# Performance work log

Measured on AMD Instinct MI355X. Metric: run time of the kernel, lower is better.

Reference implementation:

```python
import jax, jax.numpy as jnp
import numpy as np

C3_CONNECTIONS = [[0, 1, 2], [1, 2, 3], [2, 3, 4], [3, 4, 5], [4, 5, 0], [5, 0, 1],
                  [0, 1, 2, 3], [1, 2, 3, 4], [2, 3, 4, 5], [3, 4, 5, 0], [4, 5, 0, 1], [5, 0, 1, 2],
                  [0, 1, 3, 4], [1, 2, 4, 5], [0, 2, 3, 5], [0, 1, 2, 3, 4, 5]]

def _connectivity_mask():
    # [16, 6, 5, 5] binary mask encoding the partial-connection table
    m = np.zeros((16, 6, 5, 5), dtype=np.float32)
    for i, conn in enumerate(C3_CONNECTIONS):
        m[i, conn] = 1.0
    return jnp.asarray(m)

MASK = _connectivity_mask()


def setup_inputs() -> dict:
    key = jax.random.key(0)
    kx, kw, kb = jax.random.split(key, 3)
    x = jax.random.normal(kx, (64, 6, 256, 256), dtype=jnp.float32)
    # full dense weight; unconnected entries are masked out inside reference(),
    # which makes the math identical to the 16 separate tiny convs
    W = jax.random.normal(kw, (16, 6, 5, 5), dtype=jnp.float32) * 0.1
    b = jax.random.normal(kb, (16,), dtype=jnp.float32) * 0.1
    return {"x": x, "W": W, "b": b}


def reference(x, W, b):
    # masked dense conv == 16 channel-subset convs concatenated on channel dim
    Wm = W * MASK
    y = jax.lax.conv_general_dilated(
        x, Wm, window_strides=(1, 1), padding='VALID',
        dimension_numbers=('NCHW', 'OIHW', 'NCHW'))
    y = y + b[None, :, None, None]  # [B, 16, 252, 252]
    return 1.7159 * jnp.tanh((2.0 / 3.0) * y)
```

## Files before the change

### kernel.cpp

```cpp
#include <hip/hip_runtime.h>


__device__ __forceinline__ void conv25(const float* __restrict__ wp,
                                       const float (&win)[6][5],
                                       float& a0, float& a1) {
    #pragma unroll
    for (int ky = 0; ky < 5; ++ky)
        #pragma unroll
        for (int kx = 0; kx < 5; ++kx) {
            const float wv = wp[ky * 5 + kx];
            a0 = fmaf(win[ky + 0][kx], wv, a0);
            a1 = fmaf(win[ky + 1][kx], wv, a1);
        }
}

__global__ __launch_bounds__(256) void c3_partial_conv_kernel(
    const float* __restrict__ x,
    const float* __restrict__ W,
    const float* __restrict__ b,
    float* __restrict__ out)
{
    constexpr int G0N[6] = {4, 5, 5, 5, 4, 3};
    constexpr int G0O[6][5] = {
        {0, 4, 5, 6, 0},
        {0, 1, 5, 6, 7},
        {0, 1, 2, 6, 7},
        {1, 2, 3, 6, 7},
        {2, 3, 4, 7, 0},
        {3, 4, 5, 0, 0}};
    constexpr int G1N[6] = {6, 5, 5, 5, 6, 7};
    constexpr int G1O[6][7] = {
        {9, 10, 11, 12, 14, 15, 8},
        {10, 11, 12, 13, 15, 8, 8},
        {8, 11, 13, 14, 15, 8, 8},
        {8, 9, 12, 14, 15, 8, 8},
        {8, 9, 10, 12, 13, 15, 8},
        {8, 9, 10, 11, 13, 14, 15}};

    __shared__ float lds[6][20][40];

    const int tx  = threadIdx.x;
    const int ty  = threadIdx.y;
    const int tid = ty * 32 + tx;

    const int tileX = blockIdx.x << 5;
    const int tileY = blockIdx.y << 4;
    const int batch = blockIdx.z;

    const float* xb = x + (size_t)batch * 6 * 256 * 256;

    for (int i = tid; i < 1080; i += 256) {
        int c   = i / 180;
        int rem = i - c * 180;
        int r   = rem / 9;
        int q   = rem - r * 9;
        int gr  = tileY + r;
        int gc0 = tileX + (q << 2);
        float4 v = make_float4(0.f, 0.f, 0.f, 0.f);
        if (gr < 256 && gc0 < 256)
            v = *reinterpret_cast<const float4*>(&xb[(c * 256 + gr) * 256 + gc0]);
        *reinterpret_cast<float4*>(&lds[c][r][q << 2]) = v;
    }
    __syncthreads();

    const int row0 = ty << 1;
    const int ocol = tileX + tx;
    float* ob = out + (size_t)batch * 16 * 252 * 252;
    const bool colok = (ocol < 252);

    {
        float acc[8][2];
        #pragma unroll
        for (int o = 0; o < 8; ++o) {
            float bv = b[o];
            acc[o][0] = bv; acc[o][1] = bv;
        }

        #pragma unroll 1
        for (int c = 0; c < 6; ++c) {
            float win[6][5];
            #pragma unroll
            for (int r = 0; r < 6; ++r)
                #pragma unroll
                for (int j = 0; j < 5; ++j) {
                    win[r][j] = lds[c][row0 + r][tx + j];
                    asm volatile("" : "+v"(win[r][j]));
                }

            const int n = G0N[c];
            #pragma unroll 1
            for (int oi = 0; oi < n; ++oi) {
                switch (G0O[c][oi]) {
                    case 0: conv25(W + (0 * 6 + c) * 25, win, acc[0][0], acc[0][1]); break;
                    case 1: conv25(W + (1 * 6 + c) * 25, win, acc[1][0], acc[1][1]); break;
                    case 2: conv25(W + (2 * 6 + c) * 25, win, acc[2][0], acc[2][1]); break;
                    case 3: conv25(W + (3 * 6 + c) * 25, win, acc[3][0], acc[3][1]); break;
                    case 4: conv25(W + (4 * 6 + c) * 25, win, acc[4][0], acc[4][1]); break;
                    case 5: conv25(W + (5 * 6 + c) * 25, win, acc[5][0], acc[5][1]); break;
                    case 6: conv25(W + (6 * 6 + c) * 25, win, acc[6][0], acc[6][1]); break;
                    case 7: conv25(W + (7 * 6 + c) * 25, win, acc[7][0], acc[7][1]); break;
                    default: break;
                }
            }
        }

        if (colok) {
            #pragma unroll
            for (int o = 0; o < 8; ++o)
                #pragma unroll
                for (int dy = 0; dy < 2; ++dy) {
                    int orow = tileY + row0 + dy;
                    if (orow < 252) {
                        float z = acc[o][dy] * (2.0f / 3.0f);
                        float e = __expf(2.0f * z);
                        float rr = __builtin_amdgcn_rcpf(e + 1.0f);
                        ob[(o * 252 + orow) * 252 + ocol] = 1.7159f * (1.0f - 2.0f * rr);
                    }
                }
        }
    }

    __builtin_amdgcn_sched_barrier(0);

    {
        float acc[8][2];
        #pragma unroll
        for (int o = 0; o < 8; ++o) {
            float bv = b[8 + o];
            acc[o][0] = bv; acc[o][1] = bv;
        }

        #pragma unroll 1
        for (int c = 0; c < 6; ++c) {
            float win[6][5];
            #pragma unroll
            for (int r = 0; r < 6; ++r)
                #pragma unroll
                for (int j = 0; j < 5; ++j) {
                    win[r][j] = lds[c][row0 + r][tx + j];
                    asm volatile("" : "+v"(win[r][j]));
                }

            const int n = G1N[c];
            #pragma unroll 1
            for (int oi = 0; oi < n; ++oi) {
                switch (G1O[c][oi]) {
                    case  8: conv25(W + ( 8 * 6 + c) * 25, win, acc[0][0], acc[0][1]); break;
                    case  9: conv25(W + ( 9 * 6 + c) * 25, win, acc[1][0], acc[1][1]); break;
                    case 10: conv25(W + (10 * 6 + c) * 25, win, acc[2][0], acc[2][1]); break;
                    case 11: conv25(W + (11 * 6 + c) * 25, win, acc[3][0], acc[3][1]); break;
                    case 12: conv25(W + (12 * 6 + c) * 25, win, acc[4][0], acc[4][1]); break;
                    case 13: conv25(W + (13 * 6 + c) * 25, win, acc[5][0], acc[5][1]); break;
                    case 14: conv25(W + (14 * 6 + c) * 25, win, acc[6][0], acc[6][1]); break;
                    case 15: conv25(W + (15 * 6 + c) * 25, win, acc[7][0], acc[7][1]); break;
                    default: break;
                }
            }
        }

        if (colok) {
            #pragma unroll
            for (int o = 0; o < 8; ++o)
                #pragma unroll
                for (int dy = 0; dy < 2; ++dy) {
                    int orow = tileY + row0 + dy;
                    if (orow < 252) {
                        float z = acc[o][dy] * (2.0f / 3.0f);
                        float e = __expf(2.0f * z);
                        float rr = __builtin_amdgcn_rcpf(e + 1.0f);
                        ob[((8 + o) * 252 + orow) * 252 + ocol] = 1.7159f * (1.0f - 2.0f * rr);
                    }
                }
        }
    }
}

extern "C" void kernel_launch(void* const* d_in, const int* in_sizes, int n_in,
                              void* d_out, int out_size, void* d_ws, size_t ws_size,
                              hipStream_t stream) {
    const float* x = (const float*)d_in[0];
    const float* W = (const float*)d_in[1];
    const float* b = (const float*)d_in[2];
    float* out = (float*)d_out;

    dim3 grid(8, 16, 64);
    dim3 block(32, 8);
    hipLaunchKernelGGL(c3_partial_conv_kernel, grid, block, 0, stream, x, W, b, out);
}
```

Baseline: 252.8 us.

## Pack row pairs in LDS and use packed FMA with duplicated weights

Shared memory now stores each input as interleaved pairs of adjacent rows (v2f). This lets each thread compute its two output rows with packed two-wide FMAs (v_pk_fma_f32) against weights that a small prep kernel duplicates and pads into a workspace. The goal is to halve the FMA instruction count and the scalar LDS reads per window. It adds a second kernel launch, a workspace dependency, doubled LDS footprint per pixel, and two accumulator chains merged at the end.

```diff
diff --git a/kernel.cpp b/kernel.cpp
--- a/kernel.cpp
+++ b/kernel.cpp
@@ -1,22 +1,33 @@
 #include <hip/hip_runtime.h>
 
 
-__device__ __forceinline__ void conv25(const float* __restrict__ wp,
-                                       const float (&win)[6][5],
-                                       float& a0, float& a1) {
+typedef float v2f __attribute__((ext_vector_type(2)));
+
+__global__ void prep_weights(const float* __restrict__ W, float* __restrict__ Wp) {
+    int i = blockIdx.x * 256 + threadIdx.x;
+    if (i < 96 * 64) {
+        int oc = i >> 6, k = i & 63;
+        Wp[i] = (k < 50) ? W[oc * 25 + (k >> 1)] : 0.0f;
+    }
+}
+
+__device__ __forceinline__ void convpk(const v2f* __restrict__ w2,
+                                       const v2f (&win)[5][5], v2f& acc) {
+    v2f t0 = acc;
+    v2f t1 = {0.0f, 0.0f};
     #pragma unroll
     for (int ky = 0; ky < 5; ++ky)
         #pragma unroll
         for (int kx = 0; kx < 5; ++kx) {
-            const float wv = wp[ky * 5 + kx];
-            a0 = fmaf(win[ky + 0][kx], wv, a0);
-            a1 = fmaf(win[ky + 1][kx], wv, a1);
-        }
+            if (ky & 1) t1 = __builtin_elementwise_fma(win[ky][kx], w2[ky * 5 + kx], t1);
+            else        t0 = __builtin_elementwise_fma(win[ky][kx], w2[ky * 5 + kx], t0);
+        }
+    acc = t0 + t1;
 }
 
 __global__ __launch_bounds__(256) void c3_partial_conv_kernel(
     const float* __restrict__ x,
-    const float* __restrict__ W,
+    const float* __restrict__ Wp,
     const float* __restrict__ b,
     float* __restrict__ out)
 {
@@ -37,7 +48,7 @@
         {8, 9, 10, 12, 13, 15, 8},
         {8, 9, 10, 11, 13, 14, 15}};
 
-    __shared__ float lds[6][20][40];
+    __shared__ v2f ldsP[6][19][40];
 
     const int tx  = threadIdx.x;
     const int ty  = threadIdx.y;
@@ -49,17 +60,25 @@
 
     const float* xb = x + (size_t)batch * 6 * 256 * 256;
 
-    for (int i = tid; i < 1080; i += 256) {
-        int c   = i / 180;
-        int rem = i - c * 180;
-        int r   = rem / 9;
-        int q   = rem - r * 9;
-        int gr  = tileY + r;
+    for (int i = tid; i < 1026; i += 256) {
+        int c   = i / 171;
+        int rem = i - c * 171;
+        int pr  = rem / 9;
+        int q   = rem - pr * 9;
+        int gr  = tileY + pr;
         int gc0 = tileX + (q << 2);
-        float4 v = make_float4(0.f, 0.f, 0.f, 0.f);
-        if (gr < 256 && gc0 < 256)
-            v = *reinterpret_cast<const float4*>(&xb[(c * 256 + gr) * 256 + gc0]);
-        *reinterpret_cast<float4*>(&lds[c][r][q << 2]) = v;
+        float4 a = make_float4(0.f, 0.f, 0.f, 0.f);
+        float4 d = make_float4(0.f, 0.f, 0.f, 0.f);
+        if (gc0 < 256) {
+            const float* rowp = &xb[(c * 256 + gr) * 256 + gc0];
+            if (gr < 256)     a = *reinterpret_cast<const float4*>(rowp);
+            if (gr + 1 < 256) d = *reinterpret_cast<const float4*>(rowp + 256);
+        }
+        v2f* dst = &ldsP[c][pr][q << 2];
+        dst[0] = v2f{a.x, d.x};
+        dst[1] = v2f{a.y, d.y};
+        dst[2] = v2f{a.z, d.z};
+        dst[3] = v2f{a.w, d.w};
     }
     __syncthreads();
 
@@ -67,38 +86,36 @@
     const int ocol = tileX + tx;
     float* ob = out + (size_t)batch * 16 * 252 * 252;
     const bool colok = (ocol < 252);
+    const v2f* w2base = reinterpret_cast<const v2f*>(Wp);
 
     {
-        float acc[8][2];
+        v2f accp[8];
         #pragma unroll
-        for (int o = 0; o < 8; ++o) {
-            float bv = b[o];
-            acc[o][0] = bv; acc[o][1] = bv;
-        }
+        for (int o = 0; o < 8; ++o) { float bv = b[o]; accp[o] = v2f{bv, bv}; }
 
         #pragma unroll 1
         for (int c = 0; c < 6; ++c) {
-            float win[6][5];
-            #pragma unroll
-            for (int r = 0; r < 6; ++r)
-                #pragma unroll
-                for (int j = 0; j < 5; ++j) {
-                    win[r][j] = lds[c][row0 + r][tx + j];
-                    asm volatile("" : "+v"(win[r][j]));
-                }
+            v2f win[5][5];
+            const v2f* cb = &ldsP[c][row0][tx];
+            #pragma unroll
+            for (int ky = 0; ky < 5; ++ky)
+                #pragma unroll
+                for (int kx = 0; kx < 5; ++kx)
+                    win[ky][kx] = cb[ky * 40 + kx];
 
             const int n = G0N[c];
             #pragma unroll 1
             for (int oi = 0; oi < n; ++oi) {
-                switch (G0O[c][oi]) {
-                    case 0: conv25(W + (0 * 6 + c) * 25, win, acc[0][0], acc[0][1]); break;
-                    case 1: conv25(W + (1 * 6 + c) * 25, win, acc[1][0], acc[1][1]); break;
-                    case 2: conv25(W + (2 * 6 + c) * 25, win, acc[2][0], acc[2][1]); break;
-                    case 3: conv25(W + (3 * 6 + c) * 25, win, acc[3][0], acc[3][1]); break;
-                    case 4: conv25(W + (4 * 6 + c) * 25, win, acc[4][0], acc[4][1]); break;
-                    case 5: conv25(W + (5 * 6 + c) * 25, win, acc[5][0], acc[5][1]); break;
-                    case 6: conv25(W + (6 * 6 + c) * 25, win, acc[6][0], acc[6][1]); break;
-                    case 7: conv25(W + (7 * 6 + c) * 25, win, acc[7][0], acc[7][1]); break;
+                const int o = G0O[c][oi];
+                switch (o) {
+                    case 0: convpk(w2base + (0 * 6 + c) * 32, win, accp[0]); break;
+                    case 1: convpk(w2base + (1 * 6 + c) * 32, win, accp[1]); break;
+                    case 2: convpk(w2base + (2 * 6 + c) * 32, win, accp[2]); break;
+                    case 3: convpk(w2base + (3 * 6 + c) * 32, win, accp[3]); break;
+                    case 4: convpk(w2base + (4 * 6 + c) * 32, win, accp[4]); break;
+                    case 5: convpk(w2base + (5 * 6 + c) * 32, win, accp[5]); break;
+                    case 6: convpk(w2base + (6 * 6 + c) * 32, win, accp[6]); break;
+                    case 7: convpk(w2base + (7 * 6 + c) * 32, win, accp[7]); break;
                     default: break;
                 }
             }
@@ -106,53 +123,52 @@
 
         if (colok) {
             #pragma unroll
-            for (int o = 0; o < 8; ++o)
+            for (int o = 0; o < 8; ++o) {
+                float av[2] = {accp[o].x, accp[o].y};
                 #pragma unroll
                 for (int dy = 0; dy < 2; ++dy) {
                     int orow = tileY + row0 + dy;
                     if (orow < 252) {
-                        float z = acc[o][dy] * (2.0f / 3.0f);
+                        float z = av[dy] * (2.0f / 3.0f);
                         float e = __expf(2.0f * z);
                         float rr = __builtin_amdgcn_rcpf(e + 1.0f);
                         ob[(o * 252 + orow) * 252 + ocol] = 1.7159f * (1.0f - 2.0f * rr);
                     }
                 }
+            }
         }
     }
 
     __builtin_amdgcn_sched_barrier(0);
 
     {
-        float acc[8][2];
+        v2f accp[8];
         #pragma unroll
-        for (int o = 0; o < 8; ++o) {
-            float bv = b[8 + o];
-            acc[o][0] = bv; acc[o][1] = bv;
-        }
+        for (int o = 0; o < 8; ++o) { float bv = b[8 + o]; accp[o] = v2f{bv, bv}; }
 
         #pragma unroll 1
         for (int c = 0; c < 6; ++c) {
-            float win[6][5];
-            #pragma unroll
-            for (int r = 0; r < 6; ++r)
-                #pragma unroll
-                for (int j = 0; j < 5; ++j) {
-                    win[r][j] = lds[c][row0 + r][tx + j];
-                    asm volatile("" : "+v"(win[r][j]));
-                }
+            v2f win[5][5];
+            const v2f* cb = &ldsP[c][row0][tx];
+            #pragma unroll
+            for (int ky = 0; ky < 5; ++ky)
+                #pragma unroll
+                for (int kx = 0; kx < 5; ++kx)
+                    win[ky][kx] = cb[ky * 40 + kx];
 
             const int n = G1N[c];
             #pragma unroll 1
             for (int oi = 0; oi < n; ++oi) {
-                switch (G1O[c][oi]) {
-                    case  8: conv25(W + ( 8 * 6 + c) * 25, win, acc[0][0], acc[0][1]); break;
-                    case  9: conv25(W + ( 9 * 6 + c) * 25, win, acc[1][0], acc[1][1]); break;
-                    case 10: conv25(W + (10 * 6 + c) * 25, win, acc[2][0], acc[2][1]); break;
-                    case 11: conv25(W + (11 * 6 + c) * 25, win, acc[3][0], acc[3][1]); break;
-                    case 12: conv25(W + (12 * 6 + c) * 25, win, acc[4][0], acc[4][1]); break;
-                    case 13: conv25(W + (13 * 6 + c) * 25, win, acc[5][0], acc[5][1]); break;
-                    case 14: conv25(W + (14 * 6 + c) * 25, win, acc[6][0], acc[6][1]); break;
-                    case 15: conv25(W + (15 * 6 + c) * 25, win, acc[7][0], acc[7][1]); break;
+                const int o = G1O[c][oi];
+                switch (o) {
+                    case  8: convpk(w2base + ( 8 * 6 + c) * 32, win, accp[0]); break;
+                    case  9: convpk(w2base + ( 9 * 6 + c) * 32, win, accp[1]); break;
+                    case 10: convpk(w2base + (10 * 6 + c) * 32, win, accp[2]); break;
+                    case 11: convpk(w2base + (11 * 6 + c) * 32, win, accp[3]); break;
+                    case 12: convpk(w2base + (12 * 6 + c) * 32, win, accp[4]); break;
+                    case 13: convpk(w2base + (13 * 6 + c) * 32, win, accp[5]); break;
+                    case 14: convpk(w2base + (14 * 6 + c) * 32, win, accp[6]); break;
+                    case 15: convpk(w2base + (15 * 6 + c) * 32, win, accp[7]); break;
                     default: break;
                 }
             }
@@ -160,17 +176,19 @@
 
         if (colok) {
             #pragma unroll
-            for (int o = 0; o < 8; ++o)
+            for (int o = 0; o < 8; ++o) {
+                float av[2] = {accp[o].x, accp[o].y};
                 #pragma unroll
                 for (int dy = 0; dy < 2; ++dy) {
                     int orow = tileY + row0 + dy;
                     if (orow < 252) {
-                        float z = acc[o][dy] * (2.0f / 3.0f);
+                        float z = av[dy] * (2.0f / 3.0f);
                         float e = __expf(2.0f * z);
                         float rr = __builtin_amdgcn_rcpf(e + 1.0f);
                         ob[((8 + o) * 252 + orow) * 252 + ocol] = 1.7159f * (1.0f - 2.0f * rr);
                     }
                 }
+            }
         }
     }
 }
@@ -182,8 +200,11 @@
     const float* W = (const float*)d_in[1];
     const float* b = (const float*)d_in[2];
     float* out = (float*)d_out;
+    float* Wp  = (float*)d_ws;
+
+    hipLaunchKernelGGL(prep_weights, dim3(24), dim3(256), 0, stream, W, Wp);
 
     dim3 grid(8, 16, 64);
     dim3 block(32, 8);
-    hipLaunchKernelGGL(c3_partial_conv_kernel, grid, block, 0, stream, x, W, b, out);
-}
+    hipLaunchKernelGGL(c3_partial_conv_kernel, grid, block, 0, stream, x, Wp, b, out);
+}
```

New measurement: 282.1 us. 1.12x slower.
